# Optimization experiments

Hardware: AMD Instinct MI355X
Metric: run time of the kernel (lower is better)

## Reference

```python
import jax, jax.numpy as jnp
import numpy as np

B, T, E, H = 2, 2048, 768, 12
HD = E // H  # 64


def setup_inputs() -> dict:
    key = jax.random.key(0)
    ks = jax.random.split(key, 5)
    s = 0.02
    return {
        "token_embeddings": jax.random.normal(ks[0], (B, T, E), dtype=jnp.float32),
        "W_Q": jax.random.normal(ks[1], (E, E), dtype=jnp.float32) * s,
        "W_K": jax.random.normal(ks[2], (E, E), dtype=jnp.float32) * s,
        "W_V": jax.random.normal(ks[3], (E, E), dtype=jnp.float32) * s,
        "W_pool": jax.random.normal(ks[4], (E, E), dtype=jnp.float32) * s,
    }


def reference(token_embeddings, W_Q, W_K, W_V, W_pool):
    # torch Linear (bias=False): y = x @ W.T with W of shape (out, in)
    Q = token_embeddings @ W_Q.T
    K = token_embeddings @ W_K.T
    V = token_embeddings @ W_V.T
    # Faithful replication of the module's unusual head split:
    # contiguous view (B, T, E) -> (B, H, T, HD), NOT the standard split+transpose.
    Q = Q.reshape(B, H, T, HD)
    K = K.reshape(B, H, T, HD)
    V = V.reshape(B, H, T, HD)
    scores = jnp.einsum("bhqd,bhkd->bhqk", Q, K)  # [B,H,T,T]
    causal = jnp.tril(jnp.ones((T, T), dtype=bool))
    scores = jnp.where(causal, scores, -jnp.inf)
    attn = jax.nn.softmax(scores / jnp.float32(np.sqrt(HD)), axis=-1)
    out = jnp.einsum("bhqk,bhkd->bhqd", attn, V)  # [B,H,T,HD]
    # Faithful: transpose(1,2) then contiguous view back to (B, T, E)
    out = jnp.transpose(out, (0, 2, 1, 3)).reshape(B, T, E)
    return out @ W_pool.T
```

## Files before the change

kernel.cpp:

```cpp
#include <hip/hip_runtime.h>

typedef unsigned short u16;
typedef unsigned int u32;
typedef __attribute__((ext_vector_type(8))) short bf16x8;
typedef __attribute__((ext_vector_type(4))) float f32x4;
typedef __attribute__((ext_vector_type(4))) unsigned short u16x4;
typedef __attribute__((ext_vector_type(2))) unsigned int u32x2;

#define GM 4096
#define GN 768
#define GK 768
#define NITEMS 768

static __device__ __forceinline__ u16 f2bf(float f) {
  union { float f; unsigned u; } v; v.f = f;
  unsigned u = v.u;
  return (u16)((u + 0x7FFFu + ((u >> 16) & 1u)) >> 16);
}

static __device__ __forceinline__ u32 pack_bf16(float lo, float hi) {
  return (u32)f2bf(lo) | ((u32)f2bf(hi) << 16);
}

static __device__ __forceinline__ void gld16(const void* g, void* l) {
  __builtin_amdgcn_global_load_lds((__attribute__((address_space(1))) void*)(g),
                                   (__attribute__((address_space(3))) void*)(l),
                                   16, 0, 0);
}

__global__ void cvt_bf16(const float* __restrict__ in, u16* __restrict__ out, int n4) {
  int i = blockIdx.x * blockDim.x + threadIdx.x;
  if (i < n4) {
    float4 v = ((const float4*)in)[i];
    u16x4 o;
    o[0] = f2bf(v.x); o[1] = f2bf(v.y); o[2] = f2bf(v.z); o[3] = f2bf(v.w);
    ((u16x4*)out)[i] = o;
  }
}

__global__ void cvt_w4(const float* __restrict__ w0, const float* __restrict__ w1,
                       const float* __restrict__ w2, const float* __restrict__ w3,
                       u16* __restrict__ o0, u16* __restrict__ o1,
                       u16* __restrict__ o2, u16* __restrict__ o3, int n4) {
  const float* in = blockIdx.y == 0 ? w0 : (blockIdx.y == 1 ? w1 : (blockIdx.y == 2 ? w2 : w3));
  u16* out = blockIdx.y == 0 ? o0 : (blockIdx.y == 1 ? o1 : (blockIdx.y == 2 ? o2 : o3));
  int i = blockIdx.x * blockDim.x + threadIdx.x;
  if (i < n4) {
    float4 v = ((const float4*)in)[i];
    u16x4 o;
    o[0] = f2bf(v.x); o[1] = f2bf(v.y); o[2] = f2bf(v.z); o[3] = f2bf(v.w);
    ((u16x4*)out)[i] = o;
  }
}

template<int F32OUT>
static __device__ __forceinline__ void gemm_core(const u16* __restrict__ A,
                                                 const u16* __restrict__ B,
                                                 void* __restrict__ O,
                                                 u16* lA, u16* lB)
{
  const int tid = threadIdx.x;
  const int wave = tid >> 6, lane = tid & 63;
  const int g = lane >> 4, c = lane & 15;
  const int wr = (wave >> 1) * 64, wc = (wave & 1) * 64;
  const int tm = blockIdx.x * 128, tn = blockIdx.y * 128;

  f32x4 acc[4][4] = {};

  const int srow = lane >> 2;
  const int scolb = (lane & 3) * 16;
  const char* gA = (const char*)(A + (size_t)tm * GK);
  const char* gB = (const char*)(B + (size_t)tn * GK);

  for (int k0 = 0; k0 < GK; k0 += 32) {
#pragma unroll
    for (int i = 0; i < 2; ++i) {
      const int chunk = wave * 2 + i;
      const int row = chunk * 16 + srow;
      gld16(gA + (size_t)row * (GK * 2) + k0 * 2 + scolb, (char*)lA + chunk * 1024);
      gld16(gB + (size_t)row * (GK * 2) + k0 * 2 + scolb, (char*)lB + chunk * 1024);
    }
    __syncthreads();
    bf16x8 af[4], bfr[4];
#pragma unroll
    for (int m = 0; m < 4; ++m)
      af[m] = *(const bf16x8*)((const char*)lA + (wr + m * 16 + c) * 64 + g * 16);
#pragma unroll
    for (int n = 0; n < 4; ++n)
      bfr[n] = *(const bf16x8*)((const char*)lB + (wc + n * 16 + c) * 64 + g * 16);
#pragma unroll
    for (int m = 0; m < 4; ++m)
#pragma unroll
      for (int n = 0; n < 4; ++n)
        acc[m][n] = __builtin_amdgcn_mfma_f32_16x16x32_bf16(af[m], bfr[n], acc[m][n], 0, 0, 0);
    __syncthreads();
  }

#pragma unroll
  for (int m = 0; m < 4; ++m)
#pragma unroll
    for (int n = 0; n < 4; ++n) {
      const int row0 = tm + wr + m * 16 + g * 4;
      const int col = tn + wc + n * 16 + c;
#pragma unroll
      for (int r = 0; r < 4; ++r) {
        if (F32OUT)
          ((float*)O)[(size_t)(row0 + r) * GN + col] = acc[m][n][r];
        else
          ((u16*)O)[(size_t)(row0 + r) * GN + col] = f2bf(acc[m][n][r]);
      }
    }
}

__global__ __launch_bounds__(256) void gemm_qkv(const u16* __restrict__ A,
    const u16* __restrict__ B0, const u16* __restrict__ B1, const u16* __restrict__ B2,
    u16* __restrict__ O0, u16* __restrict__ O1, u16* __restrict__ O2)
{
  __shared__ u16 lA[4096], lB[4096];
  const u16* B = blockIdx.z == 0 ? B0 : (blockIdx.z == 1 ? B1 : B2);
  u16* O = blockIdx.z == 0 ? O0 : (blockIdx.z == 1 ? O1 : O2);
  gemm_core<0>(A, B, O, lA, lB);
}

__global__ __launch_bounds__(256) void gemm_pool(const u16* __restrict__ A,
    const u16* __restrict__ B, float* __restrict__ O)
{
  __shared__ u16 lA[4096], lB[4096];
  gemm_core<1>(A, B, O, lA, lB);
}

__global__ __launch_bounds__(256) void vtrans(const u16* __restrict__ V, u16* __restrict__ VT) {
  const int tblk = blockIdx.x;
  const int bh = blockIdx.y;
  __shared__ u16 tile[64][72];
  const u16* Vh = V + (size_t)bh * 131072;
  u16* Vt = VT + (size_t)bh * 131072;
  const int tid = threadIdx.x;
  const int t0 = tblk * 64;
#pragma unroll
  for (int i = 0; i < 4; ++i) {
    int idx = i * 256 + tid;
    int row = idx >> 4;
    int c4 = idx & 15;
    u16x4 v = *(const u16x4*)(Vh + (size_t)(t0 + row) * 64 + c4 * 4);
    tile[row][c4 * 4 + 0] = v[0]; tile[row][c4 * 4 + 1] = v[1];
    tile[row][c4 * 4 + 2] = v[2]; tile[row][c4 * 4 + 3] = v[3];
  }
  __syncthreads();
#pragma unroll
  for (int i = 0; i < 4; ++i) {
    int idx = i * 256 + tid;
    int d = idx >> 4;
    int t4 = idx & 15;
    u16x4 o;
    o[0] = tile[t4 * 4 + 0][d]; o[1] = tile[t4 * 4 + 1][d];
    o[2] = tile[t4 * 4 + 2][d]; o[3] = tile[t4 * 4 + 3][d];
    *(u16x4*)(Vt + (size_t)d * 2048 + t0 + t4 * 4) = o;
  }
}

static __device__ __forceinline__ void stage_tile(const char* gbase, int rowstride,
                                                  char* lbuf, int wave, int lane) {
#pragma unroll
  for (int i = 0; i < 2; ++i) {
    const int chunk = i * 256 + wave * 64 + lane;
    const int row = chunk >> 3;
    const int colb = (chunk & 7) << 4;
    const char* src = gbase + (size_t)row * rowstride + (colb ^ ((row & 7) << 4));
    char* dst = lbuf + i * 4096 + wave * 1024;
    gld16(src, dst);
  }
}

__global__ __launch_bounds__(256, 4) void attn(const u16* __restrict__ Q,
                                               const u16* __restrict__ Km,
                                               const u16* __restrict__ VT,
                                               u16* __restrict__ X2,
                                               u32* __restrict__ qcount)
{
  const int tid = threadIdx.x, wave = tid >> 6, lane = tid & 63;
  const int g = lane >> 4, c = lane & 15;
  const int swr = (c & 7) << 4;
  const int swz = ((c & 7) ^ (c >> 3)) << 4;

  __shared__ char Kl[2][8192];
  __shared__ char Vl[2][8192];
  __shared__ u16 Plds[4][1024];
  __shared__ int s_item;
  u16* pl = Plds[wave];

  for (;;) {
    if (tid == 0) s_item = (int)atomicAdd(qcount, 1u);
    __syncthreads();
    const int w = s_item;
    if (w >= NITEMS) return;
    const int qblk = 31 - (w / 24);
    const int bh = w % 24;
    const int b = bh / 12, h = bh % 12;

    const char* Khb = (const char*)(Km + (size_t)bh * 131072);
    const char* Vhb = (const char*)(VT + (size_t)bh * 131072);
    const u16* Qh = Q + (size_t)bh * 131072;

    const int q0 = qblk * 64 + wave * 16;
    const int nkt = qblk + 1;

    stage_tile(Khb, 128, Kl[0], wave, lane);
    stage_tile(Vhb, 4096, Vl[0], wave, lane);

    bf16x8 qf[2];
#pragma unroll
    for (int kk = 0; kk < 2; ++kk)
      qf[kk] = *(const bf16x8*)(Qh + (size_t)(q0 + c) * 64 + kk * 32 + g * 8);

    f32x4 oacc[4] = {};
    float lsum = 0.f;

    __syncthreads();

    for (int kt = 0; kt < nkt; ++kt) {
      const int cur = kt & 1;
      if (kt + 1 < nkt) {
        stage_tile(Khb + (size_t)(kt + 1) * 8192, 128, Kl[cur ^ 1], wave, lane);
        stage_tile(Vhb + (size_t)(kt + 1) * 128, 4096, Vl[cur ^ 1], wave, lane);
      }
      f32x4 s[4] = {};
      __builtin_amdgcn_s_setprio(1);
#pragma unroll
      for (int kk = 0; kk < 2; ++kk)
#pragma unroll
        for (int n = 0; n < 4; ++n) {
          bf16x8 kf = *(const bf16x8*)(Kl[cur] + (size_t)(n * 16 + c) * 128 + ((kk * 64 + g * 16) ^ swr));
          s[n] = __builtin_amdgcn_mfma_f32_16x16x32_bf16(kf, qf[kk], s[n], 0, 0, 0);
        }
      __builtin_amdgcn_s_setprio(0);
      if (kt == nkt - 1) {
        const int qrow = q0 + c;
#pragma unroll
        for (int n = 0; n < 4; ++n) {
          const int k0i = kt * 64 + n * 16 + g * 4;
          float p0 = (k0i + 0 > qrow) ? 0.f : __expf(s[n][0] * 0.125f);
          float p1 = (k0i + 1 > qrow) ? 0.f : __expf(s[n][1] * 0.125f);
          float p2 = (k0i + 2 > qrow) ? 0.f : __expf(s[n][2] * 0.125f);
          float p3 = (k0i + 3 > qrow) ? 0.f : __expf(s[n][3] * 0.125f);
          lsum += (p0 + p1) + (p2 + p3);
          u32x2 pw; pw[0] = pack_bf16(p0, p1); pw[1] = pack_bf16(p2, p3);
          *(u32x2*)((char*)pl + c * 128 + ((n * 32 + g * 8) ^ swz)) = pw;
        }
      } else {
#pragma unroll
        for (int n = 0; n < 4; ++n) {
          float p0 = __expf(s[n][0] * 0.125f);
          float p1 = __expf(s[n][1] * 0.125f);
          float p2 = __expf(s[n][2] * 0.125f);
          float p3 = __expf(s[n][3] * 0.125f);
          lsum += (p0 + p1) + (p2 + p3);
          u32x2 pw; pw[0] = pack_bf16(p0, p1); pw[1] = pack_bf16(p2, p3);
          *(u32x2*)((char*)pl + c * 128 + ((n * 32 + g * 8) ^ swz)) = pw;
        }
      }
      __builtin_amdgcn_s_setprio(1);
#pragma unroll
      for (int kk = 0; kk < 2; ++kk) {
        bf16x8 pa = *(const bf16x8*)((const char*)pl + c * 128 + ((kk * 64 + g * 16) ^ swz));
#pragma unroll
        for (int n = 0; n < 4; ++n) {
          bf16x8 vf = *(const bf16x8*)(Vl[cur] + (size_t)(n * 16 + c) * 128 + ((kk * 64 + g * 16) ^ swr));
          oacc[n] = __builtin_amdgcn_mfma_f32_16x16x32_bf16(pa, vf, oacc[n], 0, 0, 0);
        }
      }
      __builtin_amdgcn_s_setprio(0);
      __syncthreads();
    }

    float tot = lsum;
    tot += __shfl_xor(tot, 16);
    tot += __shfl_xor(tot, 32);
    float linv[4];
#pragma unroll
    for (int r = 0; r < 4; ++r)
      linv[r] = __frcp_rn(__shfl(tot, g * 4 + r));
#pragma unroll
    for (int n = 0; n < 4; ++n)
#pragma unroll
      for (int r = 0; r < 4; ++r) {
        const float o = oacc[n][r] * linv[r];
        const int t = q0 + g * 4 + r;
        X2[((size_t)b * 2048 + t) * 768 + h * 64 + n * 16 + c] = f2bf(o);
      }
  }
}

extern "C" void kernel_launch(void* const* d_in, const int* in_sizes, int n_in,
                              void* d_out, int out_size, void* d_ws, size_t ws_size,
                              hipStream_t stream) {
  const float* x  = (const float*)d_in[0];
  const float* wq = (const float*)d_in[1];
  const float* wk = (const float*)d_in[2];
  const float* wv = (const float*)d_in[3];
  const float* wp = (const float*)d_in[4];

  const size_t SZ_X = (size_t)GM * GN * 2;
  const size_t SZ_W = (size_t)GK * GN * 2;
  char* ws = (char*)d_ws;
  u16* xbf  = (u16*)(ws);
  u16* wqb  = (u16*)(ws + SZ_X);
  u16* wkb  = (u16*)(ws + SZ_X + SZ_W);
  u16* wvb  = (u16*)(ws + SZ_X + 2 * SZ_W);
  u16* wpb  = (u16*)(ws + SZ_X + 3 * SZ_W);
  u16* Qb   = (u16*)(ws + SZ_X + 4 * SZ_W);
  u16* Kb   = (u16*)(ws + 2 * SZ_X + 4 * SZ_W);
  u16* Vb   = (u16*)(ws + 3 * SZ_X + 4 * SZ_W);
  u16* VT   = (u16*)(ws + 4 * SZ_X + 4 * SZ_W);
  u16* X2   = (u16*)(ws + 5 * SZ_X + 4 * SZ_W);
  u32* qcount = (u32*)(ws + 6 * SZ_X + 4 * SZ_W);
  if (ws_size < 6 * SZ_X + 4 * SZ_W + 256) return;

  cvt_bf16<<<dim3(3072), dim3(256), 0, stream>>>(x, xbf, GM * GN / 4);
  cvt_w4<<<dim3(576, 4), dim3(256), 0, stream>>>(wq, wk, wv, wp, wqb, wkb, wvb, wpb, GK * GN / 4);
  hipMemsetAsync(qcount, 0, sizeof(u32), stream);

  gemm_qkv<<<dim3(32, 6, 3), dim3(256), 0, stream>>>(xbf, wqb, wkb, wvb, Qb, Kb, Vb);
  vtrans<<<dim3(32, 24), dim3(256), 0, stream>>>(Vb, VT);
  attn<<<dim3(768), dim3(256), 0, stream>>>(Qb, Kb, VT, X2, qcount);
  gemm_pool<<<dim3(32, 6), dim3(256), 0, stream>>>(X2, wpb, (float*)d_out);
}
```

Baseline: 109.0 us.

## Fold softmax scale into Q projection, use raw exp2, prefetch V fragments

The softmax scale times log2(e) is folded into the Q projection epilogue, so the attention loop calls the hardware v_exp_f32 directly with no per-element multiply and no __expf range handling. The bf16 packing is simplified to a round-half-up bias add that drops the tie-to-even term. V fragments are loaded from LDS before the exp phase so their latency overlaps with the softmax math. This costs a little accuracy (Q rounded after scaling, and slightly different rounding ties) and raises register pressure from holding eight V fragments.

```diff
diff --git a/kernel.cpp b/kernel.cpp
--- a/kernel.cpp
+++ b/kernel.cpp
@@ -11,6 +11,7 @@
 #define GN 768
 #define GK 768
 #define NITEMS 768
+#define QSCALE 0.18033688011112042f
 
 static __device__ __forceinline__ u16 f2bf(float f) {
   union { float f; unsigned u; } v; v.f = f;
@@ -18,8 +19,16 @@
   return (u16)((u + 0x7FFFu + ((u >> 16) & 1u)) >> 16);
 }
 
-static __device__ __forceinline__ u32 pack_bf16(float lo, float hi) {
-  return (u32)f2bf(lo) | ((u32)f2bf(hi) << 16);
+static __device__ __forceinline__ float exp2_hw(float x) {
+  float r;
+  asm("v_exp_f32 %0, %1" : "=v"(r) : "v"(x));
+  return r;
+}
+
+static __device__ __forceinline__ u32 pack_rn(float lo, float hi) {
+  u32 a = __float_as_uint(lo) + 0x8000u;
+  u32 b = __float_as_uint(hi) + 0x8000u;
+  return (a >> 16) | (b & 0xFFFF0000u);
 }
 
 static __device__ __forceinline__ void gld16(const void* g, void* l) {
@@ -57,7 +66,7 @@
 static __device__ __forceinline__ void gemm_core(const u16* __restrict__ A,
                                                  const u16* __restrict__ B,
                                                  void* __restrict__ O,
-                                                 u16* lA, u16* lB)
+                                                 u16* lA, u16* lB, float scale)
 {
   const int tid = threadIdx.x;
   const int wave = tid >> 6, lane = tid & 63;
@@ -107,7 +116,7 @@
         if (F32OUT)
           ((float*)O)[(size_t)(row0 + r) * GN + col] = acc[m][n][r];
         else
-          ((u16*)O)[(size_t)(row0 + r) * GN + col] = f2bf(acc[m][n][r]);
+          ((u16*)O)[(size_t)(row0 + r) * GN + col] = f2bf(acc[m][n][r] * scale);
       }
     }
 }
@@ -119,14 +128,15 @@
   __shared__ u16 lA[4096], lB[4096];
   const u16* B = blockIdx.z == 0 ? B0 : (blockIdx.z == 1 ? B1 : B2);
   u16* O = blockIdx.z == 0 ? O0 : (blockIdx.z == 1 ? O1 : O2);
-  gemm_core<0>(A, B, O, lA, lB);
+  const float scale = blockIdx.z == 0 ? QSCALE : 1.0f;
+  gemm_core<0>(A, B, O, lA, lB, scale);
 }
 
 __global__ __launch_bounds__(256) void gemm_pool(const u16* __restrict__ A,
     const u16* __restrict__ B, float* __restrict__ O)
 {
   __shared__ u16 lA[4096], lB[4096];
-  gemm_core<1>(A, B, O, lA, lB);
+  gemm_core<1>(A, B, O, lA, lB, 1.0f);
 }
 
 __global__ __launch_bounds__(256) void vtrans(const u16* __restrict__ V, u16* __restrict__ VT) {
@@ -234,28 +244,34 @@
           s[n] = __builtin_amdgcn_mfma_f32_16x16x32_bf16(kf, qf[kk], s[n], 0, 0, 0);
         }
       __builtin_amdgcn_s_setprio(0);
+      bf16x8 vf[2][4];
+#pragma unroll
+      for (int kk = 0; kk < 2; ++kk)
+#pragma unroll
+        for (int n = 0; n < 4; ++n)
+          vf[kk][n] = *(const bf16x8*)(Vl[cur] + (size_t)(n * 16 + c) * 128 + ((kk * 64 + g * 16) ^ swr));
       if (kt == nkt - 1) {
         const int qrow = q0 + c;
 #pragma unroll
         for (int n = 0; n < 4; ++n) {
           const int k0i = kt * 64 + n * 16 + g * 4;
-          float p0 = (k0i + 0 > qrow) ? 0.f : __expf(s[n][0] * 0.125f);
-          float p1 = (k0i + 1 > qrow) ? 0.f : __expf(s[n][1] * 0.125f);
-          float p2 = (k0i + 2 > qrow) ? 0.f : __expf(s[n][2] * 0.125f);
-          float p3 = (k0i + 3 > qrow) ? 0.f : __expf(s[n][3] * 0.125f);
+          float p0 = (k0i + 0 > qrow) ? 0.f : exp2_hw(s[n][0]);
+          float p1 = (k0i + 1 > qrow) ? 0.f : exp2_hw(s[n][1]);
+          float p2 = (k0i + 2 > qrow) ? 0.f : exp2_hw(s[n][2]);
+          float p3 = (k0i + 3 > qrow) ? 0.f : exp2_hw(s[n][3]);
           lsum += (p0 + p1) + (p2 + p3);
-          u32x2 pw; pw[0] = pack_bf16(p0, p1); pw[1] = pack_bf16(p2, p3);
+          u32x2 pw; pw[0] = pack_rn(p0, p1); pw[1] = pack_rn(p2, p3);
           *(u32x2*)((char*)pl + c * 128 + ((n * 32 + g * 8) ^ swz)) = pw;
         }
       } else {
 #pragma unroll
         for (int n = 0; n < 4; ++n) {
-          float p0 = __expf(s[n][0] * 0.125f);
-          float p1 = __expf(s[n][1] * 0.125f);
-          float p2 = __expf(s[n][2] * 0.125f);
-          float p3 = __expf(s[n][3] * 0.125f);
+          float p0 = exp2_hw(s[n][0]);
+          float p1 = exp2_hw(s[n][1]);
+          float p2 = exp2_hw(s[n][2]);
+          float p3 = exp2_hw(s[n][3]);
           lsum += (p0 + p1) + (p2 + p3);
-          u32x2 pw; pw[0] = pack_bf16(p0, p1); pw[1] = pack_bf16(p2, p3);
+          u32x2 pw; pw[0] = pack_rn(p0, p1); pw[1] = pack_rn(p2, p3);
           *(u32x2*)((char*)pl + c * 128 + ((n * 32 + g * 8) ^ swz)) = pw;
         }
       }
@@ -264,10 +280,8 @@
       for (int kk = 0; kk < 2; ++kk) {
         bf16x8 pa = *(const bf16x8*)((const char*)pl + c * 128 + ((kk * 64 + g * 16) ^ swz));
 #pragma unroll
-        for (int n = 0; n < 4; ++n) {
-          bf16x8 vf = *(const bf16x8*)(Vl[cur] + (size_t)(n * 16 + c) * 128 + ((kk * 64 + g * 16) ^ swr));
-          oacc[n] = __builtin_amdgcn_mfma_f32_16x16x32_bf16(pa, vf, oacc[n], 0, 0, 0);
-        }
+        for (int n = 0; n < 4; ++n)
+          oacc[n] = __builtin_amdgcn_mfma_f32_16x16x32_bf16(pa, vf[kk][n], oacc[n], 0, 0, 0);
       }
       __builtin_amdgcn_s_setprio(0);
       __syncthreads();
```

Result: faster. 105.2 us (-3.5%).
